# Performance work log

Hardware: AMD Instinct MI355X
Metric: run time of the kernel (lower is better)

Reference implementation:

```python
import jax, jax.numpy as jnp
import numpy as np

B, T, DIM, HID, E = 2, 4096, 1024, 512, 16


def setup_inputs() -> dict:
    key = jax.random.key(0)
    k1, k2, k3, k4 = jax.random.split(key, 4)
    x = jax.random.normal(k1, (B, T, DIM), jnp.float32)
    w1 = jax.random.normal(k2, (E, HID, DIM), jnp.float32) * 0.02
    w2 = jax.random.normal(k3, (E, DIM, HID), jnp.float32) * 0.02
    w3 = jax.random.normal(k4, (E, HID, DIM), jnp.float32) * 0.02
    # Random integer partition of T per batch row: variable-size expert groups
    rng = np.random.default_rng(0)
    cuts = np.sort(rng.integers(0, T, size=(B, E - 1)), axis=1)
    bounds = np.concatenate([np.zeros((B, 1), np.int64), cuts, np.full((B, 1), T, np.int64)], axis=1)
    counts = jnp.asarray(np.diff(bounds, axis=1), jnp.int32)  # [B, E], rows sum to T
    return {"x": x, "num_tokens_per_expert": counts, "w1": w1, "w2": w2, "w3": w3}


def reference(x, num_tokens_per_expert, w1, w2, w3):
    # offsets[b, e] = end of expert e's contiguous token slice in row b
    offsets = jnp.cumsum(num_tokens_per_expert, axis=1).astype(jnp.int32)  # [B, E]
    tok = jnp.arange(x.shape[1])
    # expert owning each token position (tokens are pre-grouped per expert)
    expert_id = jax.vmap(lambda o: jnp.searchsorted(o, tok, side='right'))(offsets)  # [B, T]

    xb = x.astype(jnp.bfloat16)

    def body(acc, scanned):
        e, w1e, w2e, w3e = scanned
        h = jax.nn.silu(xb @ w1e.T) * (xb @ w3e.T)        # [B, T, HID] bf16 SwiGLU
        y = h @ w2e.T                                      # [B, T, DIM]
        acc = acc + jnp.where((expert_id == e)[..., None], y, jnp.bfloat16(0))
        return acc, None

    nE = w1.shape[0]
    acc0 = jnp.zeros(x.shape, jnp.bfloat16)
    out, _ = jax.lax.scan(
        body, acc0,
        (jnp.arange(nE), w1.astype(jnp.bfloat16), w2.astype(jnp.bfloat16), w3.astype(jnp.bfloat16)))
    return out.astype(x.dtype)
```

## Files before the change

### kernel.cpp

```cpp
#include <hip/hip_runtime.h>
#include <hip/hip_bf16.h>
#include <stdint.h>

#define Bq   2
#define Tq   4096
#define DIMq 1024
#define HIDq 512
#define Eq   16
#define Mq   (Bq * Tq)

typedef __attribute__((ext_vector_type(8))) short bf16x8;
typedef __attribute__((ext_vector_type(4))) float f32x4;
typedef unsigned long long ull;

__device__ __forceinline__ unsigned int f2bf(float f) {
  unsigned int u = __builtin_bit_cast(unsigned int, f);
  return (u + 0x7FFFu + ((u >> 16) & 1u)) >> 16;
}
__device__ __forceinline__ float bf2f(unsigned int s) {
  unsigned int u = s << 16;
  return __builtin_bit_cast(float, u);
}
__device__ __forceinline__ ull pack4(const float4 v) {
  return (ull)f2bf(v.x)
       | ((ull)f2bf(v.y) << 16)
       | ((ull)f2bf(v.z) << 32)
       | ((ull)f2bf(v.w) << 48);
}

#define GLOAD16(gp, lp)                                                        \
  __builtin_amdgcn_global_load_lds(                                            \
      (const __attribute__((address_space(1))) unsigned int*)(gp),             \
      (__attribute__((address_space(3))) unsigned int*)(lp), 16, 0, 0)

__global__ __launch_bounds__(256) void convert4_kernel(
    const float* __restrict__ x,  const float* __restrict__ w1,
    const float* __restrict__ w2, const float* __restrict__ w3,
    ull* __restrict__ xb, ull* __restrict__ w1b,
    ull* __restrict__ w2b, ull* __restrict__ w3b) {
  const float* s;
  ull* d;
  switch (blockIdx.y) {
    case 0:  s = x;  d = xb;  break;
    case 1:  s = w1; d = w1b; break;
    case 2:  s = w2; d = w2b; break;
    default: s = w3; d = w3b; break;
  }
  const int N4 = (8388608 / 4);
  for (int i = blockIdx.x * blockDim.x + threadIdx.x; i < N4;
       i += gridDim.x * blockDim.x) {
    float4 v = ((const float4*)s)[i];
    d[i] = pack4(v);
  }
}

__global__ void setup_kernel(const int* __restrict__ counts, int* __restrict__ seg_off) {
  int b = blockIdx.x;
  if (threadIdx.x == 0) {
    int s = 0;
    seg_off[b * (Eq + 1)] = 0;
    for (int e = 0; e < Eq; ++e) {
      s += counts[b * Eq + e];
      seg_off[b * (Eq + 1) + e + 1] = s;
    }
  }
}

__device__ __forceinline__ void chunk_decode(int bid, int& mt, int& nt) {
  const int c = bid & 7;
  const int k = bid >> 3;
  mt = c * 8 + (k >> 3);
  nt = k & 7;
}

__global__ __launch_bounds__(256) void gemm1_kernel(
    const unsigned short* __restrict__ xb, const unsigned short* __restrict__ w1b,
    const unsigned short* __restrict__ w3b, const int* __restrict__ seg_off,
    unsigned short* __restrict__ hbuf) {
  int mt, nt;
  chunk_decode(blockIdx.x, mt, nt);
  const int t0  = mt * 128;
  const int n0  = nt * 64;
  const int b   = t0 >> 12;
  const int tl0 = t0 & (Tq - 1);

  __shared__ unsigned short As[2][128 * 64];
  __shared__ unsigned short W1s[2][64 * 64];
  __shared__ unsigned short W3s[2][64 * 64];

  const int tid  = threadIdx.x;
  const int lane = tid & 63;
  const int wv   = tid >> 6;
  const int wm2  = (wv >> 1) * 64;
  const int wn2  = (wv & 1) * 32;
  const int q    = lane >> 4;
  const int l15  = lane & 15;
  const int rsw  = (l15 & 7) << 4;

  #pragma unroll 1
  for (int e = 0; e < Eq; ++e) {
    const int lo = seg_off[b * (Eq + 1) + e];
    const int hi = seg_off[b * (Eq + 1) + e + 1];
    const int s  = lo > tl0 ? lo : tl0;
    const int en = hi < tl0 + 128 ? hi : tl0 + 128;
    if (s >= en) continue;

    const unsigned short* __restrict__ w1e = w1b + (size_t)e * HIDq * DIMq;
    const unsigned short* __restrict__ w3e = w3b + (size_t)e * HIDq * DIMq;

    f32x4 acc1[4][2], acc3[4][2];
    #pragma unroll
    for (int i = 0; i < 4; ++i)
      #pragma unroll
      for (int j = 0; j < 2; ++j) { acc1[i][j] = (f32x4)0.f; acc3[i][j] = (f32x4)0.f; }

    auto stage = [&](int k0, int bi) {
      #pragma unroll
      for (int it = 0; it < 4; ++it) {
        const int c = it * 256 + tid;
        const int row = c >> 3;
        const int kc = ((c & 7) << 3) ^ ((row & 7) << 3);
        GLOAD16(xb + (size_t)(t0 + row) * DIMq + k0 + kc,
                (char*)&As[bi][0] + it * 4096 + wv * 1024);
      }
      #pragma unroll
      for (int it = 0; it < 2; ++it) {
        const int c = it * 256 + tid;
        const int row = c >> 3;
        const int kc = ((c & 7) << 3) ^ ((row & 7) << 3);
        GLOAD16(w1e + (size_t)(n0 + row) * DIMq + k0 + kc,
                (char*)&W1s[bi][0] + it * 4096 + wv * 1024);
        GLOAD16(w3e + (size_t)(n0 + row) * DIMq + k0 + kc,
                (char*)&W3s[bi][0] + it * 4096 + wv * 1024);
      }
    };
    auto compute = [&](int bi) {
      const char* Ab = (const char*)&As[bi][0];
      const char* Ub = (const char*)&W1s[bi][0];
      const char* Vb = (const char*)&W3s[bi][0];
      #pragma unroll
      for (int ks = 0; ks < 2; ++ks) {
        const int kb = (ks * 64 + q * 16) ^ rsw;
        bf16x8 a[4], u[2], v[2];
        #pragma unroll
        for (int i = 0; i < 4; ++i)
          a[i] = *(const bf16x8*)(Ab + (wm2 + i * 16 + l15) * 128 + kb);
        #pragma unroll
        for (int j = 0; j < 2; ++j) {
          u[j] = *(const bf16x8*)(Ub + (wn2 + j * 16 + l15) * 128 + kb);
          v[j] = *(const bf16x8*)(Vb + (wn2 + j * 16 + l15) * 128 + kb);
        }
        #pragma unroll
        for (int i = 0; i < 4; ++i)
          #pragma unroll
          for (int j = 0; j < 2; ++j) {
            acc1[i][j] = __builtin_amdgcn_mfma_f32_16x16x32_bf16(a[i], u[j], acc1[i][j], 0, 0, 0);
            acc3[i][j] = __builtin_amdgcn_mfma_f32_16x16x32_bf16(a[i], v[j], acc3[i][j], 0, 0, 0);
          }
      }
    };

    stage(0, 0);
    __syncthreads();
    int cur = 0;
    #pragma unroll 1
    for (int k0 = 0; k0 < DIMq; k0 += 64) {
      if (k0 + 64 < DIMq) stage(k0 + 64, cur ^ 1);
      compute(cur);
      __syncthreads();
      cur ^= 1;
    }

    const int rlo = s - tl0, rhi = en - tl0;
    #pragma unroll
    for (int i = 0; i < 4; ++i)
      #pragma unroll
      for (int j = 0; j < 2; ++j)
        #pragma unroll
        for (int rr = 0; rr < 4; ++rr) {
          const int row = wm2 + i * 16 + q * 4 + rr;
          if (row >= rlo && row < rhi) {
            const float aa = bf2f(f2bf(acc1[i][j][rr]));
            const float cc = bf2f(f2bf(acc3[i][j][rr]));
            const float sg = bf2f(f2bf(1.f / (1.f + __expf(-aa))));
            const float tt = bf2f(f2bf(aa * sg));
            hbuf[(size_t)(t0 + row) * HIDq + n0 + wn2 + j * 16 + l15] =
                (unsigned short)f2bf(tt * cc);
          }
        }
  }
}

__global__ __launch_bounds__(256) void gemm2_kernel(
    const unsigned short* __restrict__ hb, const unsigned short* __restrict__ w2b,
    const int* __restrict__ seg_off, float* __restrict__ out) {
  int mt, nt;
  chunk_decode(blockIdx.x, mt, nt);
  const int t0  = mt * 128;
  const int n0  = nt * 128;
  const int b   = t0 >> 12;
  const int tl0 = t0 & (Tq - 1);

  __shared__ unsigned short Hs[2][128 * 64];
  __shared__ unsigned short Bs[2][128 * 64];

  const int tid  = threadIdx.x;
  const int lane = tid & 63;
  const int wv   = tid >> 6;
  const int wm2  = (wv >> 1) * 64;
  const int wn2  = (wv & 1) * 64;
  const int q    = lane >> 4;
  const int l15  = lane & 15;
  const int rsw  = (l15 & 7) << 4;

  #pragma unroll 1
  for (int e = 0; e < Eq; ++e) {
    const int lo = seg_off[b * (Eq + 1) + e];
    const int hi = seg_off[b * (Eq + 1) + e + 1];
    const int s  = lo > tl0 ? lo : tl0;
    const int en = hi < tl0 + 128 ? hi : tl0 + 128;
    if (s >= en) continue;

    const unsigned short* __restrict__ w2e = w2b + (size_t)e * DIMq * HIDq;

    f32x4 acc[4][4];
    #pragma unroll
    for (int i = 0; i < 4; ++i)
      #pragma unroll
      for (int j = 0; j < 4; ++j) acc[i][j] = (f32x4)0.f;

    auto stage = [&](int k0, int bi) {
      #pragma unroll
      for (int it = 0; it < 4; ++it) {
        const int c = it * 256 + tid;
        const int row = c >> 3;
        const int kc = ((c & 7) << 3) ^ ((row & 7) << 3);
        GLOAD16(hb + (size_t)(t0 + row) * HIDq + k0 + kc,
                (char*)&Hs[bi][0] + it * 4096 + wv * 1024);
        GLOAD16(w2e + (size_t)(n0 + row) * HIDq + k0 + kc,
                (char*)&Bs[bi][0] + it * 4096 + wv * 1024);
      }
    };
    auto compute = [&](int bi) {
      const char* Ab = (const char*)&Hs[bi][0];
      const char* Wb = (const char*)&Bs[bi][0];
      #pragma unroll
      for (int ks = 0; ks < 2; ++ks) {
        const int kb = (ks * 64 + q * 16) ^ rsw;
        bf16x8 a[4], w[4];
        #pragma unroll
        for (int i = 0; i < 4; ++i) {
          a[i] = *(const bf16x8*)(Ab + (wm2 + i * 16 + l15) * 128 + kb);
          w[i] = *(const bf16x8*)(Wb + (wn2 + i * 16 + l15) * 128 + kb);
        }
        #pragma unroll
        for (int i = 0; i < 4; ++i)
          #pragma unroll
          for (int j = 0; j < 4; ++j)
            acc[i][j] = __builtin_amdgcn_mfma_f32_16x16x32_bf16(a[i], w[j], acc[i][j], 0, 0, 0);
      }
    };

    stage(0, 0);
    __syncthreads();
    int cur = 0;
    #pragma unroll 1
    for (int k0 = 0; k0 < HIDq; k0 += 64) {
      if (k0 + 64 < HIDq) stage(k0 + 64, cur ^ 1);
      compute(cur);
      __syncthreads();
      cur ^= 1;
    }

    const int rlo = s - tl0, rhi = en - tl0;
    #pragma unroll
    for (int i = 0; i < 4; ++i)
      #pragma unroll
      for (int j = 0; j < 4; ++j)
        #pragma unroll
        for (int rr = 0; rr < 4; ++rr) {
          const int row = wm2 + i * 16 + q * 4 + rr;
          if (row >= rlo && row < rhi) {
            out[(size_t)(t0 + row) * DIMq + n0 + wn2 + j * 16 + l15] =
                bf2f(f2bf(acc[i][j][rr]));
          }
        }
  }
}

extern "C" void kernel_launch(void* const* d_in, const int* in_sizes, int n_in,
                              void* d_out, int out_size, void* d_ws, size_t ws_size,
                              hipStream_t stream) {
  const float* x      = (const float*)d_in[0];
  const int*   counts = (const int*)d_in[1];
  const float* w1     = (const float*)d_in[2];
  const float* w2     = (const float*)d_in[3];
  const float* w3     = (const float*)d_in[4];
  float* out = (float*)d_out;

  char* ws = (char*)d_ws;
  int* seg_off = (int*)ws;
  unsigned short* xb  = (unsigned short*)(ws + 256);
  unsigned short* w1b = (unsigned short*)(ws + 256 + (16u << 20));
  unsigned short* w2b = (unsigned short*)(ws + 256 + (32u << 20));
  unsigned short* w3b = (unsigned short*)(ws + 256 + (48u << 20));
  unsigned short* hb  = (unsigned short*)(ws + 256 + (64u << 20));

  convert4_kernel<<<dim3(2048, 4), 256, 0, stream>>>(
      x, w1, w2, w3, (ull*)xb, (ull*)w1b, (ull*)w2b, (ull*)w3b);
  setup_kernel<<<dim3(Bq), 64, 0, stream>>>(counts, seg_off);
  gemm1_kernel<<<512, 256, 0, stream>>>(xb, w1b, w3b, seg_off, hb);
  gemm2_kernel<<<512, 256, 0, stream>>>(hb, w2b, seg_off, out);
}
```

Measured before the change: 280.7 us.

## Use 8 waves per GEMM block and fold segment offsets into kernels

Both grouped GEMM kernels now launch 512 threads (8 waves) per 128-row tile, each wave owning 32 rows instead of 64. This halves per-wave accumulators and gives each CU more waves for latency hiding. The setup kernel is removed and each GEMM block computes the expert prefix sums inline from counts, saving one launch. The trade-off is smaller per-wave MFMA tiles, which means more LDS reads per FLOP and more barrier participants.

```diff
diff --git a/kernel.cpp b/kernel.cpp
--- a/kernel.cpp
+++ b/kernel.cpp
@@ -54,18 +54,6 @@
   }
 }
 
-__global__ void setup_kernel(const int* __restrict__ counts, int* __restrict__ seg_off) {
-  int b = blockIdx.x;
-  if (threadIdx.x == 0) {
-    int s = 0;
-    seg_off[b * (Eq + 1)] = 0;
-    for (int e = 0; e < Eq; ++e) {
-      s += counts[b * Eq + e];
-      seg_off[b * (Eq + 1) + e + 1] = s;
-    }
-  }
-}
-
 __device__ __forceinline__ void chunk_decode(int bid, int& mt, int& nt) {
   const int c = bid & 7;
   const int k = bid >> 3;
@@ -73,9 +61,9 @@
   nt = k & 7;
 }
 
-__global__ __launch_bounds__(256) void gemm1_kernel(
+__global__ __launch_bounds__(512) void gemm1_kernel(
     const unsigned short* __restrict__ xb, const unsigned short* __restrict__ w1b,
-    const unsigned short* __restrict__ w3b, const int* __restrict__ seg_off,
+    const unsigned short* __restrict__ w3b, const int* __restrict__ counts,
     unsigned short* __restrict__ hbuf) {
   int mt, nt;
   chunk_decode(blockIdx.x, mt, nt);
@@ -91,47 +79,46 @@
   const int tid  = threadIdx.x;
   const int lane = tid & 63;
   const int wv   = tid >> 6;
-  const int wm2  = (wv >> 1) * 64;
+  const int wm2  = (wv >> 1) * 32;
   const int wn2  = (wv & 1) * 32;
   const int q    = lane >> 4;
   const int l15  = lane & 15;
   const int rsw  = (l15 & 7) << 4;
 
+  int lo = 0;
   #pragma unroll 1
   for (int e = 0; e < Eq; ++e) {
-    const int lo = seg_off[b * (Eq + 1) + e];
-    const int hi = seg_off[b * (Eq + 1) + e + 1];
+    const int hi = lo + counts[b * Eq + e];
     const int s  = lo > tl0 ? lo : tl0;
     const int en = hi < tl0 + 128 ? hi : tl0 + 128;
+    lo = hi;
     if (s >= en) continue;
 
     const unsigned short* __restrict__ w1e = w1b + (size_t)e * HIDq * DIMq;
     const unsigned short* __restrict__ w3e = w3b + (size_t)e * HIDq * DIMq;
 
-    f32x4 acc1[4][2], acc3[4][2];
+    f32x4 acc1[2][2], acc3[2][2];
     #pragma unroll
-    for (int i = 0; i < 4; ++i)
+    for (int i = 0; i < 2; ++i)
       #pragma unroll
       for (int j = 0; j < 2; ++j) { acc1[i][j] = (f32x4)0.f; acc3[i][j] = (f32x4)0.f; }
 
     auto stage = [&](int k0, int bi) {
       #pragma unroll
-      for (int it = 0; it < 4; ++it) {
-        const int c = it * 256 + tid;
+      for (int it = 0; it < 2; ++it) {
+        const int c = it * 512 + tid;
         const int row = c >> 3;
         const int kc = ((c & 7) << 3) ^ ((row & 7) << 3);
         GLOAD16(xb + (size_t)(t0 + row) * DIMq + k0 + kc,
-                (char*)&As[bi][0] + it * 4096 + wv * 1024);
-      }
-      #pragma unroll
-      for (int it = 0; it < 2; ++it) {
-        const int c = it * 256 + tid;
-        const int row = c >> 3;
-        const int kc = ((c & 7) << 3) ^ ((row & 7) << 3);
+                (char*)&As[bi][0] + it * 8192 + wv * 1024);
+      }
+      {
+        const int row = tid >> 3;
+        const int kc = ((tid & 7) << 3) ^ ((row & 7) << 3);
         GLOAD16(w1e + (size_t)(n0 + row) * DIMq + k0 + kc,
-                (char*)&W1s[bi][0] + it * 4096 + wv * 1024);
+                (char*)&W1s[bi][0] + wv * 1024);
         GLOAD16(w3e + (size_t)(n0 + row) * DIMq + k0 + kc,
-                (char*)&W3s[bi][0] + it * 4096 + wv * 1024);
+                (char*)&W3s[bi][0] + wv * 1024);
       }
     };
     auto compute = [&](int bi) {
@@ -141,9 +128,9 @@
       #pragma unroll
       for (int ks = 0; ks < 2; ++ks) {
         const int kb = (ks * 64 + q * 16) ^ rsw;
-        bf16x8 a[4], u[2], v[2];
-        #pragma unroll
-        for (int i = 0; i < 4; ++i)
+        bf16x8 a[2], u[2], v[2];
+        #pragma unroll
+        for (int i = 0; i < 2; ++i)
           a[i] = *(const bf16x8*)(Ab + (wm2 + i * 16 + l15) * 128 + kb);
         #pragma unroll
         for (int j = 0; j < 2; ++j) {
@@ -151,7 +138,7 @@
           v[j] = *(const bf16x8*)(Vb + (wn2 + j * 16 + l15) * 128 + kb);
         }
         #pragma unroll
-        for (int i = 0; i < 4; ++i)
+        for (int i = 0; i < 2; ++i)
           #pragma unroll
           for (int j = 0; j < 2; ++j) {
             acc1[i][j] = __builtin_amdgcn_mfma_f32_16x16x32_bf16(a[i], u[j], acc1[i][j], 0, 0, 0);
@@ -173,7 +160,7 @@
 
     const int rlo = s - tl0, rhi = en - tl0;
     #pragma unroll
-    for (int i = 0; i < 4; ++i)
+    for (int i = 0; i < 2; ++i)
       #pragma unroll
       for (int j = 0; j < 2; ++j)
         #pragma unroll
@@ -191,9 +178,9 @@
   }
 }
 
-__global__ __launch_bounds__(256) void gemm2_kernel(
+__global__ __launch_bounds__(512) void gemm2_kernel(
     const unsigned short* __restrict__ hb, const unsigned short* __restrict__ w2b,
-    const int* __restrict__ seg_off, float* __restrict__ out) {
+    const int* __restrict__ counts, float* __restrict__ out) {
   int mt, nt;
   chunk_decode(blockIdx.x, mt, nt);
   const int t0  = mt * 128;
@@ -207,38 +194,39 @@
   const int tid  = threadIdx.x;
   const int lane = tid & 63;
   const int wv   = tid >> 6;
-  const int wm2  = (wv >> 1) * 64;
+  const int wm2  = (wv >> 1) * 32;
   const int wn2  = (wv & 1) * 64;
   const int q    = lane >> 4;
   const int l15  = lane & 15;
   const int rsw  = (l15 & 7) << 4;
 
+  int lo = 0;
   #pragma unroll 1
   for (int e = 0; e < Eq; ++e) {
-    const int lo = seg_off[b * (Eq + 1) + e];
-    const int hi = seg_off[b * (Eq + 1) + e + 1];
+    const int hi = lo + counts[b * Eq + e];
     const int s  = lo > tl0 ? lo : tl0;
     const int en = hi < tl0 + 128 ? hi : tl0 + 128;
+    lo = hi;
     if (s >= en) continue;
 
     const unsigned short* __restrict__ w2e = w2b + (size_t)e * DIMq * HIDq;
 
-    f32x4 acc[4][4];
+    f32x4 acc[2][4];
     #pragma unroll
-    for (int i = 0; i < 4; ++i)
+    for (int i = 0; i < 2; ++i)
       #pragma unroll
       for (int j = 0; j < 4; ++j) acc[i][j] = (f32x4)0.f;
 
     auto stage = [&](int k0, int bi) {
       #pragma unroll
-      for (int it = 0; it < 4; ++it) {
-        const int c = it * 256 + tid;
+      for (int it = 0; it < 2; ++it) {
+        const int c = it * 512 + tid;
         const int row = c >> 3;
         const int kc = ((c & 7) << 3) ^ ((row & 7) << 3);
         GLOAD16(hb + (size_t)(t0 + row) * HIDq + k0 + kc,
-                (char*)&Hs[bi][0] + it * 4096 + wv * 1024);
+                (char*)&Hs[bi][0] + it * 8192 + wv * 1024);
         GLOAD16(w2e + (size_t)(n0 + row) * HIDq + k0 + kc,
-                (char*)&Bs[bi][0] + it * 4096 + wv * 1024);
+                (char*)&Bs[bi][0] + it * 8192 + wv * 1024);
       }
     };
     auto compute = [&](int bi) {
@@ -247,14 +235,15 @@
       #pragma unroll
       for (int ks = 0; ks < 2; ++ks) {
         const int kb = (ks * 64 + q * 16) ^ rsw;
-        bf16x8 a[4], w[4];
-        #pragma unroll
-        for (int i = 0; i < 4; ++i) {
+        bf16x8 a[2], w[4];
+        #pragma unroll
+        for (int i = 0; i < 2; ++i)
           a[i] = *(const bf16x8*)(Ab + (wm2 + i * 16 + l15) * 128 + kb);
-          w[i] = *(const bf16x8*)(Wb + (wn2 + i * 16 + l15) * 128 + kb);
-        }
-        #pragma unroll
-        for (int i = 0; i < 4; ++i)
+        #pragma unroll
+        for (int j = 0; j < 4; ++j)
+          w[j] = *(const bf16x8*)(Wb + (wn2 + j * 16 + l15) * 128 + kb);
+        #pragma unroll
+        for (int i = 0; i < 2; ++i)
           #pragma unroll
           for (int j = 0; j < 4; ++j)
             acc[i][j] = __builtin_amdgcn_mfma_f32_16x16x32_bf16(a[i], w[j], acc[i][j], 0, 0, 0);
@@ -274,7 +263,7 @@
 
     const int rlo = s - tl0, rhi = en - tl0;
     #pragma unroll
-    for (int i = 0; i < 4; ++i)
+    for (int i = 0; i < 2; ++i)
       #pragma unroll
       for (int j = 0; j < 4; ++j)
         #pragma unroll
@@ -299,7 +288,6 @@
   float* out = (float*)d_out;
 
   char* ws = (char*)d_ws;
-  int* seg_off = (int*)ws;
   unsigned short* xb  = (unsigned short*)(ws + 256);
   unsigned short* w1b = (unsigned short*)(ws + 256 + (16u << 20));
   unsigned short* w2b = (unsigned short*)(ws + 256 + (32u << 20));
@@ -308,7 +296,6 @@
 
   convert4_kernel<<<dim3(2048, 4), 256, 0, stream>>>(
       x, w1, w2, w3, (ull*)xb, (ull*)w1b, (ull*)w2b, (ull*)w3b);
-  setup_kernel<<<dim3(Bq), 64, 0, stream>>>(counts, seg_off);
-  gemm1_kernel<<<512, 256, 0, stream>>>(xb, w1b, w3b, seg_off, hb);
-  gemm2_kernel<<<512, 256, 0, stream>>>(hb, w2b, seg_off, out);
-}
+  gemm1_kernel<<<512, 512, 0, stream>>>(xb, w1b, w3b, counts, hb);
+  gemm2_kernel<<<512, 512, 0, stream>>>(hb, w2b, counts, out);
+}
```

New measurement: 262.3 us. 1.07x faster.
